# Optimization experiments

Hardware: AMD Instinct MI355X
Metric: run time of the kernel (lower is better)

Reference implementation:

```python
import jax, jax.numpy as jnp
import numpy as np

B, T, D, H, NQ = 256, 32, 256, 256, 8


def _rx_mat(theta):
    # RX(t) = [[cos(t/2), -i sin(t/2)], [-i sin(t/2), cos(t/2)]]; theta scalar or [B]
    c = jnp.cos(theta / 2).astype(jnp.complex64)
    s = (-1j * jnp.sin(theta / 2)).astype(jnp.complex64)
    row0 = jnp.stack([c, s], axis=-1)
    row1 = jnp.stack([s, c], axis=-1)
    return jnp.stack([row0, row1], axis=-2)


def _rz_mat(theta):
    # RZ(t) = diag(e^{-it/2}, e^{+it/2})
    e = jnp.exp(-0.5j * theta).astype(jnp.complex64)
    z = jnp.zeros_like(e)
    row0 = jnp.stack([e, z], axis=-1)
    row1 = jnp.stack([z, jnp.conj(e)], axis=-1)
    return jnp.stack([row0, row1], axis=-2)


def _qlayer(angles, rx_p, rz_p, n_wires):
    # angles: [B] encoder RX angles on wire 0 (GeneralEncoder uses input_idx [0] only)
    bsz = angles.shape[0]
    dim = 1 << n_wires
    state = jnp.zeros((bsz, dim), jnp.complex64).at[:, 0].set(1.0)

    def apply1(st, mat, w):
        L = 1 << w
        s = st.reshape(bsz, L, 2, -1)  # wire w is the middle axis (wire 0 = MSB)
        if mat.ndim == 3:
            s = jnp.einsum('bij,bljr->blir', mat, s)
        else:
            s = jnp.einsum('ij,bljr->blir', mat, s)
        return s.reshape(bsz, dim)

    state = apply1(state, _rx_mat(angles), 0)  # batched encoder RX on wire 0
    for w in range(n_wires):
        state = apply1(state, _rx_mat(rx_p[w]), w)
        state = apply1(state, _rz_mat(rz_p[w]), w)
    for w in range(n_wires - 1):  # CNOT ladder, control w -> target w+1 (adjacent)
        L = 1 << w
        s = state.reshape(bsz, L, 2, 2, -1)
        s = jnp.concatenate([s[:, :, :1], s[:, :, 1:, ::-1, :]], axis=2)
        state = s.reshape(bsz, dim)
    probs = jnp.real(state * jnp.conj(state))  # [B, 2^n]
    bits = (np.arange(dim)[:, None] >> np.arange(n_wires - 1, -1, -1)[None, :]) & 1
    zmean = jnp.asarray((1.0 - 2.0 * bits).mean(axis=1), dtype=probs.dtype)
    return probs @ zmean  # mean over wires of <Z_w>, shape [B]


def _forward(inputs, Wf, bf, Wi, bi, Wg, bg, Wo, bo, rxf, rzf, rxi, rzi, rxg, rzg, rxo, rzo):
    n_wires = rxf.shape[0]
    bsz, _, d_in = inputs.shape
    hid = Wf.shape[1] - d_in
    h0 = jnp.zeros((bsz, hid), inputs.dtype)
    c0 = jnp.zeros((bsz, hid), inputs.dtype)
    xs = jnp.swapaxes(inputs, 0, 1)  # [T, B, D]

    def step(carry, x):
        hx, cx = carry
        comb = jnp.concatenate([x, hx], axis=1)

        def gate(W, b, rxp, rzp):
            ang = comb @ W.T + b  # [B, n_wires]; only column 0 feeds the encoder
            return _qlayer(ang[:, 0], rxp, rzp, n_wires)[:, None]  # [B, 1]

        f = jax.nn.sigmoid(gate(Wf, bf, rxf, rzf))
        i = jax.nn.sigmoid(gate(Wi, bi, rxi, rzi))
        g = jnp.tanh(gate(Wg, bg, rxg, rzg))
        o = jax.nn.sigmoid(gate(Wo, bo, rxo, rzo))
        cx = f * cx + i * g  # [B,1] broadcasts over hidden dim
        hx = o * jnp.tanh(cx)
        return (hx, cx), hx

    (hx, cx), ys = jax.lax.scan(step, (h0, c0), xs)
    return jnp.swapaxes(ys, 0, 1), hx, cx  # [B,T,H], [B,H], [B,H]


def setup_inputs() -> dict:
    key = jax.random.key(0)
    ks = jax.random.split(key, 18)
    scale = 1.0 / np.sqrt(D + H)
    inp = {'inputs': jax.random.normal(ks[0], (B, T, D), jnp.float32)}
    names = ['f', 'i', 'g', 'o']
    for j, n in enumerate(names):
        inp['W' + n] = jax.random.normal(ks[1 + j], (NQ, D + H), jnp.float32) * scale
        inp['b' + n] = jax.random.normal(ks[5 + j], (NQ,), jnp.float32) * scale
        inp['rx' + n] = jax.random.normal(ks[9 + j], (NQ,), jnp.float32)
        inp['rz' + n] = jax.random.normal(ks[13 + j], (NQ,), jnp.float32)
    return inp


def reference(inputs, Wf, bf, Wi, bi, Wg, bg, Wo, bo, rxf, rzf, rxi, rzi, rxg, rzg, rxo, rzo):
    return _forward(inputs, Wf, bf, Wi, bi, Wg, bg, Wo, bo,
                    rxf, rzf, rxi, rzi, rxg, rzg, rxo, rzo)
```

## Files before the change

kernel.cpp:

```cpp
#include <hip/hip_runtime.h>

#define BB 256
#define TT 32
#define DD 256
#define HH 256


__global__ __launch_bounds__(256) void qlstm_gemv(
    const float* __restrict__ x,
    const float* __restrict__ Wf, const float* __restrict__ bf,
    const float* __restrict__ Wi, const float* __restrict__ bi,
    const float* __restrict__ Wg, const float* __restrict__ bg,
    const float* __restrict__ Wo, const float* __restrict__ bo,
    float4* __restrict__ ax)
{
    const int tid  = threadIdx.x;
    const int lane = tid & 63;
    const int wave = tid >> 6;
    const int row  = blockIdx.x * 4 + wave;

    const float4 xv = reinterpret_cast<const float4*>(x + row * DD)[lane];
    const float4 wf = reinterpret_cast<const float4*>(Wf)[lane];
    const float4 wi = reinterpret_cast<const float4*>(Wi)[lane];
    const float4 wg = reinterpret_cast<const float4*>(Wg)[lane];
    const float4 wo = reinterpret_cast<const float4*>(Wo)[lane];

    float sf = xv.x*wf.x + xv.y*wf.y + xv.z*wf.z + xv.w*wf.w;
    float si = xv.x*wi.x + xv.y*wi.y + xv.z*wi.z + xv.w*wi.w;
    float sg = xv.x*wg.x + xv.y*wg.y + xv.z*wg.z + xv.w*wg.w;
    float so = xv.x*wo.x + xv.y*wo.y + xv.z*wo.z + xv.w*wo.w;

    #pragma unroll
    for (int off = 32; off > 0; off >>= 1) {
        sf += __shfl_down(sf, off);
        si += __shfl_down(si, off);
        sg += __shfl_down(sg, off);
        so += __shfl_down(so, off);
    }
    if (lane == 0)
        ax[row] = make_float4(sf + bf[0], si + bi[0], sg + bg[0], so + bo[0]);
}

__global__ __launch_bounds__(256) void qlstm_scan(
    const float* __restrict__ Wf, const float* __restrict__ rxf,
    const float* __restrict__ Wi, const float* __restrict__ rxi,
    const float* __restrict__ Wg, const float* __restrict__ rxg,
    const float* __restrict__ Wo, const float* __restrict__ rxo,
    const float* __restrict__ ax,
    float* __restrict__ hseq, float* __restrict__ hfin, float* __restrict__ cfin)
{
    __shared__ float red[256];
    __shared__ float sWh[4], sK[4], sRx0[4];
    const int tid = threadIdx.x;

    const float* Ws[4]  = {Wf, Wi, Wg, Wo};
    const float* rxs[4] = {rxf, rxi, rxg, rxo};

    for (int g = 0; g < 4; ++g) {
        red[tid] = Ws[g][DD + tid];
        __syncthreads();
        for (int s = 128; s > 0; s >>= 1) {
            if (tid < s) red[tid] += red[tid + s];
            __syncthreads();
        }
        if (tid == 0) sWh[g] = red[0];
        __syncthreads();
    }
    if (tid < 4) {
        const float* rx = rxs[tid];
        float acc = 0.f;
        for (int j = 7; j >= 1; --j) acc = cosf(rx[j]) * (1.f + acc);
        sK[tid]   = (1.f + acc) * 0.125f;
        sRx0[tid] = rx[0];
    }
    __syncthreads();

    const int g     = tid & 3;
    const int b     = blockIdx.x * 64 + (tid >> 2);
    const int lane  = tid & 63;
    const int gbase = lane & ~3;
    const float wh  = sWh[g], K = sK[g], rx0 = sRx0[g];

    float h = 0.f, c = 0.f;
    for (int t = 0; t < TT; ++t) {
        const float a  = ax[(b * TT + t) * 4 + g];
        const float v  = cosf(rx0 + a + h * wh) * K;
        const float mv = (g == 2) ? tanhf(v) : 1.f / (1.f + expf(-v));
        const float fv = __shfl(mv, gbase + 0);
        const float iv = __shfl(mv, gbase + 1);
        const float gv = __shfl(mv, gbase + 2);
        const float ov = __shfl(mv, gbase + 3);
        c = fv * c + iv * gv;
        h = ov * tanhf(c);
        if (g == 0) hseq[b * TT + t] = h;
    }
    if (g == 0) { hfin[b] = h; cfin[b] = c; }
}

__global__ __launch_bounds__(256) void qlstm_bcast(
    const float* __restrict__ hseq, const float* __restrict__ hfin,
    const float* __restrict__ cfin, float4* __restrict__ out)
{
    const int idx = blockIdx.x * 256 + threadIdx.x;
    const int e   = idx * 4;
    float v;
    if (e < BB * TT * HH)                 v = hseq[e >> 8];
    else if (e < BB * TT * HH + BB * HH)  v = hfin[(e - BB * TT * HH) >> 8];
    else                                  v = cfin[(e - BB * TT * HH - BB * HH) >> 8];
    out[idx] = make_float4(v, v, v, v);
}

extern "C" void kernel_launch(void* const* d_in, const int* in_sizes, int n_in,
                              void* d_out, int out_size, void* d_ws, size_t ws_size,
                              hipStream_t stream) {
    const float* x   = (const float*)d_in[0];
    const float* Wf  = (const float*)d_in[1];
    const float* bf  = (const float*)d_in[2];
    const float* rxf = (const float*)d_in[3];
    const float* Wi  = (const float*)d_in[5];
    const float* bi  = (const float*)d_in[6];
    const float* rxi = (const float*)d_in[7];
    const float* Wg  = (const float*)d_in[9];
    const float* bg  = (const float*)d_in[10];
    const float* rxg = (const float*)d_in[11];
    const float* Wo  = (const float*)d_in[13];
    const float* bo  = (const float*)d_in[14];
    const float* rxo = (const float*)d_in[15];

    char*   ws   = (char*)d_ws;
    float4* ax   = (float4*)ws;
    float*  hseq = (float*)(ws + 131072);
    float*  hfin = (float*)(ws + 163840);
    float*  cfin = (float*)(ws + 164864);

    qlstm_gemv<<<2048, 256, 0, stream>>>(x, Wf, bf, Wi, bi, Wg, bg, Wo, bo, ax);
    qlstm_scan<<<4, 256, 0, stream>>>(Wf, rxf, Wi, rxi, Wg, rxg, Wo, rxo,
                                      (const float*)ax, hseq, hfin, cfin);
    qlstm_bcast<<<2176, 256, 0, stream>>>(hseq, hfin, cfin, (float4*)d_out);
}
```

Baseline: 116.2 us.

## Fuse gemv, recurrent scan and broadcast into one per-batch kernel

Replaces three launches (projection gemv, 4-block scan, output broadcast) with a single kernel using one block per batch element. Each block computes its own input projections into shared memory, runs the 32-step recurrence serially on one thread, then broadcasts h/c to the output. This removes the workspace round trips and two launch gaps, and spreads the serial scan across 256 blocks instead of 4. The cost is that the recurrence runs on a single thread per block, which serialises the four gate transcendentals per step.

Result: slower. 124.5 us (+7.1%).

```diff
diff --git a/kernel.cpp b/kernel.cpp
--- a/kernel.cpp
+++ b/kernel.cpp
@@ -6,108 +6,108 @@
 #define HH 256
 
 
-__global__ __launch_bounds__(256) void qlstm_gemv(
+__global__ __launch_bounds__(256) void qlstm_fused(
     const float* __restrict__ x,
-    const float* __restrict__ Wf, const float* __restrict__ bf,
-    const float* __restrict__ Wi, const float* __restrict__ bi,
-    const float* __restrict__ Wg, const float* __restrict__ bg,
-    const float* __restrict__ Wo, const float* __restrict__ bo,
-    float4* __restrict__ ax)
+    const float* __restrict__ pWf, const float* __restrict__ pbf, const float* __restrict__ prxf,
+    const float* __restrict__ pWi, const float* __restrict__ pbi, const float* __restrict__ prxi,
+    const float* __restrict__ pWg, const float* __restrict__ pbg, const float* __restrict__ prxg,
+    const float* __restrict__ pWo, const float* __restrict__ pbo, const float* __restrict__ prxo,
+    float* __restrict__ out)
 {
+    __shared__ float sAx[TT][4];
+    __shared__ float sH[TT];
+    __shared__ float sWh[4], sK[4], sRx0[4];
+    __shared__ float sHC[2];
+
     const int tid  = threadIdx.x;
     const int lane = tid & 63;
     const int wave = tid >> 6;
-    const int row  = blockIdx.x * 4 + wave;
+    const int b    = blockIdx.x;
 
-    const float4 xv = reinterpret_cast<const float4*>(x + row * DD)[lane];
-    const float4 wf = reinterpret_cast<const float4*>(Wf)[lane];
-    const float4 wi = reinterpret_cast<const float4*>(Wi)[lane];
-    const float4 wg = reinterpret_cast<const float4*>(Wg)[lane];
-    const float4 wo = reinterpret_cast<const float4*>(Wo)[lane];
+    const float4 wf = reinterpret_cast<const float4*>(pWf)[lane];
+    const float4 wi = reinterpret_cast<const float4*>(pWi)[lane];
+    const float4 wg = reinterpret_cast<const float4*>(pWg)[lane];
+    const float4 wo = reinterpret_cast<const float4*>(pWo)[lane];
+    const float bf0 = pbf[0], bi0 = pbi[0], bg0 = pbg[0], bo0 = pbo[0];
 
-    float sf = xv.x*wf.x + xv.y*wf.y + xv.z*wf.z + xv.w*wf.w;
-    float si = xv.x*wi.x + xv.y*wi.y + xv.z*wi.z + xv.w*wi.w;
-    float sg = xv.x*wg.x + xv.y*wg.y + xv.z*wg.z + xv.w*wg.w;
-    float so = xv.x*wo.x + xv.y*wo.y + xv.z*wo.z + xv.w*wo.w;
-
-    #pragma unroll
-    for (int off = 32; off > 0; off >>= 1) {
-        sf += __shfl_down(sf, off);
-        si += __shfl_down(si, off);
-        sg += __shfl_down(sg, off);
-        so += __shfl_down(so, off);
-    }
-    if (lane == 0)
-        ax[row] = make_float4(sf + bf[0], si + bi[0], sg + bg[0], so + bo[0]);
-}
-
-__global__ __launch_bounds__(256) void qlstm_scan(
-    const float* __restrict__ Wf, const float* __restrict__ rxf,
-    const float* __restrict__ Wi, const float* __restrict__ rxi,
-    const float* __restrict__ Wg, const float* __restrict__ rxg,
-    const float* __restrict__ Wo, const float* __restrict__ rxo,
-    const float* __restrict__ ax,
-    float* __restrict__ hseq, float* __restrict__ hfin, float* __restrict__ cfin)
-{
-    __shared__ float red[256];
-    __shared__ float sWh[4], sK[4], sRx0[4];
-    const int tid = threadIdx.x;
-
-    const float* Ws[4]  = {Wf, Wi, Wg, Wo};
-    const float* rxs[4] = {rxf, rxi, rxg, rxo};
-
-    for (int g = 0; g < 4; ++g) {
-        red[tid] = Ws[g][DD + tid];
-        __syncthreads();
-        for (int s = 128; s > 0; s >>= 1) {
-            if (tid < s) red[tid] += red[tid + s];
-            __syncthreads();
-        }
-        if (tid == 0) sWh[g] = red[0];
-        __syncthreads();
+    {
+        const float* Wsel = (wave == 0) ? pWf : (wave == 1) ? pWi : (wave == 2) ? pWg : pWo;
+        const float4 hw = reinterpret_cast<const float4*>(Wsel + DD)[lane];
+        float s = hw.x + hw.y + hw.z + hw.w;
+        #pragma unroll
+        for (int off = 32; off > 0; off >>= 1) s += __shfl_down(s, off);
+        if (lane == 0) sWh[wave] = s;
     }
     if (tid < 4) {
-        const float* rx = rxs[tid];
+        const float* rx = (tid == 0) ? prxf : (tid == 1) ? prxi : (tid == 2) ? prxg : prxo;
         float acc = 0.f;
         for (int j = 7; j >= 1; --j) acc = cosf(rx[j]) * (1.f + acc);
         sK[tid]   = (1.f + acc) * 0.125f;
         sRx0[tid] = rx[0];
     }
+
+    #pragma unroll
+    for (int k = 0; k < 8; ++k) {
+        const int t = wave * 8 + k;
+        const float4 xv = reinterpret_cast<const float4*>(x + (b * TT + t) * DD)[lane];
+        float sf = xv.x*wf.x + xv.y*wf.y + xv.z*wf.z + xv.w*wf.w;
+        float si = xv.x*wi.x + xv.y*wi.y + xv.z*wi.z + xv.w*wi.w;
+        float sg = xv.x*wg.x + xv.y*wg.y + xv.z*wg.z + xv.w*wg.w;
+        float so = xv.x*wo.x + xv.y*wo.y + xv.z*wo.z + xv.w*wo.w;
+        #pragma unroll
+        for (int off = 32; off > 0; off >>= 1) {
+            sf += __shfl_down(sf, off);
+            si += __shfl_down(si, off);
+            sg += __shfl_down(sg, off);
+            so += __shfl_down(so, off);
+        }
+        if (lane == 0) {
+            sAx[t][0] = sf + bf0;
+            sAx[t][1] = si + bi0;
+            sAx[t][2] = sg + bg0;
+            sAx[t][3] = so + bo0;
+        }
+    }
     __syncthreads();
 
-    const int g     = tid & 3;
-    const int b     = blockIdx.x * 64 + (tid >> 2);
-    const int lane  = tid & 63;
-    const int gbase = lane & ~3;
-    const float wh  = sWh[g], K = sK[g], rx0 = sRx0[g];
+    if (tid == 0) {
+        const float whf = sWh[0], whi = sWh[1], whg = sWh[2], who = sWh[3];
+        const float Kf  = sK[0],  Ki  = sK[1],  Kg  = sK[2],  Ko  = sK[3];
+        const float r0f = sRx0[0], r0i = sRx0[1], r0g = sRx0[2], r0o = sRx0[3];
+        float h = 0.f, c = 0.f;
+        for (int t = 0; t < TT; ++t) {
+            const float vf = cosf(r0f + sAx[t][0] + h * whf) * Kf;
+            const float vi = cosf(r0i + sAx[t][1] + h * whi) * Ki;
+            const float vg = cosf(r0g + sAx[t][2] + h * whg) * Kg;
+            const float vo = cosf(r0o + sAx[t][3] + h * who) * Ko;
+            const float fv = 1.f / (1.f + expf(-vf));
+            const float iv = 1.f / (1.f + expf(-vi));
+            const float gv = tanhf(vg);
+            const float ov = 1.f / (1.f + expf(-vo));
+            c = fv * c + iv * gv;
+            h = ov * tanhf(c);
+            sH[t] = h;
+        }
+        sHC[0] = h; sHC[1] = c;
+    }
+    __syncthreads();
 
-    float h = 0.f, c = 0.f;
-    for (int t = 0; t < TT; ++t) {
-        const float a  = ax[(b * TT + t) * 4 + g];
-        const float v  = cosf(rx0 + a + h * wh) * K;
-        const float mv = (g == 2) ? tanhf(v) : 1.f / (1.f + expf(-v));
-        const float fv = __shfl(mv, gbase + 0);
-        const float iv = __shfl(mv, gbase + 1);
-        const float gv = __shfl(mv, gbase + 2);
-        const float ov = __shfl(mv, gbase + 3);
-        c = fv * c + iv * gv;
-        h = ov * tanhf(c);
-        if (g == 0) hseq[b * TT + t] = h;
+    float4* out4 = (float4*)out;
+    {
+        const int t = tid >> 3, j = tid & 7;
+        const float hv = sH[t];
+        const float4 h4 = make_float4(hv, hv, hv, hv);
+        const int rowb = (b * TT + t) * (HH / 4);
+        #pragma unroll
+        for (int k = 0; k < 8; ++k) out4[rowb + k * 8 + j] = h4;
     }
-    if (g == 0) { hfin[b] = h; cfin[b] = c; }
-}
-
-__global__ __launch_bounds__(256) void qlstm_bcast(
-    const float* __restrict__ hseq, const float* __restrict__ hfin,
-    const float* __restrict__ cfin, float4* __restrict__ out)
-{
-    const int idx = blockIdx.x * 256 + threadIdx.x;
-    const int e   = idx * 4;
-    float v;
-    if (e < BB * TT * HH)                 v = hseq[e >> 8];
-    else if (e < BB * TT * HH + BB * HH)  v = hfin[(e - BB * TT * HH) >> 8];
-    else                                  v = cfin[(e - BB * TT * HH - BB * HH) >> 8];
-    out[idx] = make_float4(v, v, v, v);
+    if (tid < 64) {
+        const float v = sHC[0];
+        out4[BB * TT * (HH / 4) + b * (HH / 4) + tid] = make_float4(v, v, v, v);
+    } else if (tid < 128) {
+        const float v = sHC[1];
+        out4[BB * TT * (HH / 4) + BB * (HH / 4) + b * (HH / 4) + (tid - 64)] = make_float4(v, v, v, v);
+    }
 }
 
 extern "C" void kernel_launch(void* const* d_in, const int* in_sizes, int n_in,
@@ -127,14 +127,10 @@
     const float* bo  = (const float*)d_in[14];
     const float* rxo = (const float*)d_in[15];
 
-    char*   ws   = (char*)d_ws;
-    float4* ax   = (float4*)ws;
-    float*  hseq = (float*)(ws + 131072);
-    float*  hfin = (float*)(ws + 163840);
-    float*  cfin = (float*)(ws + 164864);
-
-    qlstm_gemv<<<2048, 256, 0, stream>>>(x, Wf, bf, Wi, bi, Wg, bg, Wo, bo, ax);
-    qlstm_scan<<<4, 256, 0, stream>>>(Wf, rxf, Wi, rxi, Wg, rxg, Wo, rxo,
-                                      (const float*)ax, hseq, hfin, cfin);
-    qlstm_bcast<<<2176, 256, 0, stream>>>(hseq, hfin, cfin, (float4*)d_out);
+    qlstm_fused<<<BB, 256, 0, stream>>>(x,
+                                        Wf, bf, rxf,
+                                        Wi, bi, rxi,
+                                        Wg, bg, rxg,
+                                        Wo, bo, rxo,
+                                        (float*)d_out);
 }
```
